# Performance work log

Measured on AMD Instinct MI355X. Metric: run time of the kernel, lower is better.

The kernel has to match this reference:

```python
import jax, jax.numpy as jnp
import numpy as np

B, C, H, W = 32, 3, 224, 224
P = 14            # n_patches per side
PS = H // P       # 16
D = 768           # embed_size
NH = 12           # heads
DH = D // NH      # 64
L = 12            # n_blocks
FF = 4 * D
OUT = 1000
S = P * P + 1     # 197 tokens


def positional_encoding(seq_len, d):
    i = jnp.arange(seq_len, dtype=jnp.float32)[:, None]
    j = jnp.arange(d, dtype=jnp.float32)[None, :]
    je = jnp.where(j % 2 == 0, j, j - 1)
    ang = i / jnp.power(10000.0, je / d)
    return jnp.where(j % 2 == 0, jnp.sin(ang), jnp.cos(ang))


def layernorm(x, g, b, eps=1e-5):
    mu = jnp.mean(x, axis=-1, keepdims=True)
    var = jnp.var(x, axis=-1, keepdims=True)
    return (x - mu) * jax.lax.rsqrt(var + eps) * g + b


def setup_inputs() -> dict:
    key = jax.random.key(0)
    ks = jax.random.split(key, 20)
    s = 0.02
    inp = {
        'images': jax.random.normal(ks[0], (B, C, H, W), jnp.float32),
        'W_patch': jax.random.normal(ks[1], (D, C * PS * PS), jnp.float32) * s,
        'b_patch': jnp.zeros((D,), jnp.float32),
        'class_token': jax.random.uniform(ks[2], (1, D), jnp.float32),
        'ln1_g': jnp.ones((L, D), jnp.float32),
        'ln1_b': jnp.zeros((L, D), jnp.float32),
        'Wq': jax.random.normal(ks[3], (L, NH, DH, DH), jnp.float32) * s,
        'bq': jnp.zeros((L, NH, DH), jnp.float32),
        'Wk': jax.random.normal(ks[4], (L, NH, DH, DH), jnp.float32) * s,
        'bk': jnp.zeros((L, NH, DH), jnp.float32),
        'Wv': jax.random.normal(ks[5], (L, NH, DH, DH), jnp.float32) * s,
        'bv': jnp.zeros((L, NH, DH), jnp.float32),
        'ln2_g': jnp.ones((L, D), jnp.float32),
        'ln2_b': jnp.zeros((L, D), jnp.float32),
        'W1': jax.random.normal(ks[6], (L, FF, D), jnp.float32) * s,
        'b1': jnp.zeros((L, FF), jnp.float32),
        'W2': jax.random.normal(ks[7], (L, D, FF), jnp.float32) * s,
        'b2': jnp.zeros((L, D), jnp.float32),
        'Wo': jax.random.normal(ks[8], (OUT, D), jnp.float32) * s,
        'bo': jnp.zeros((OUT,), jnp.float32),
    }
    return inp


def reference(images, W_patch, b_patch, class_token, ln1_g, ln1_b,
              Wq, bq, Wk, bk, Wv, bv, ln2_g, ln2_b, W1, b1, W2, b2, Wo, bo):
    b = images.shape[0]
    # patch extraction: [B,C,P,ps,P,ps] -> [B,P*P, C*ps*ps] (flatten order C,h,w)
    patches = images.reshape(b, C, P, PS, P, PS).transpose(0, 2, 4, 1, 3, 5)
    patches = patches.reshape(b, P * P, C * PS * PS)
    tokens = patches @ W_patch.T + b_patch                     # [B, P^2, D]
    cls = jnp.broadcast_to(class_token[None], (b, 1, D))
    x = jnp.concatenate([cls, tokens], axis=1)                 # [B, S, D]
    x = x + positional_encoding(S, D)

    scale = 1.0 / jnp.sqrt(jnp.float32(DH))
    for l in range(L):
        h = layernorm(x, ln1_g[l], ln1_b[l])
        hh = h.reshape(b, S, NH, DH)
        q = jnp.einsum('bshd,hed->bshe', hh, Wq[l]) + bq[l]
        k = jnp.einsum('bshd,hed->bshe', hh, Wk[l]) + bk[l]
        v = jnp.einsum('bshd,hed->bshe', hh, Wv[l]) + bv[l]
        scores = jnp.einsum('bshe,bthe->bhst', q, k) * scale   # [B,H,S,S]
        attn = jax.nn.softmax(scores, axis=-1)
        o = jnp.einsum('bhst,bthe->bshe', attn, v).reshape(b, S, D)
        x = x + o
        h2 = layernorm(x, ln2_g[l], ln2_b[l])
        ff = jax.nn.gelu(h2 @ W1[l].T + b1[l], approximate=False) @ W2[l].T + b2[l]
        x = x + ff

    logits = x[:, 0] @ Wo.T + bo                               # [B, OUT]
    return jax.nn.softmax(logits, axis=-1)
```

## Files before the change

### kernel.cpp

```cpp
#include <hip/hip_runtime.h>
#include <math.h>

static constexpr int kB   = 32;
static constexpr int kC   = 3;
static constexpr int kH   = 224;
static constexpr int kW   = 224;
static constexpr int kP   = 14;
static constexpr int kPS  = 16;
static constexpr int kD   = 768;
static constexpr int kNH  = 12;
static constexpr int kDH  = 64;
static constexpr int kL   = 12;
static constexpr int kFF  = 3072;
static constexpr int kOUT = 1000;
static constexpr int kS   = 197;
static constexpr int kTOK = kB * kS;
static constexpr int kNP  = kP * kP;
static constexpr int kMP  = 6400;
static constexpr int kQKV = 3 * kD;

typedef unsigned short u16;
typedef __attribute__((ext_vector_type(4))) float f32x4;
typedef __attribute__((ext_vector_type(8))) short bf16x8;

__device__ __forceinline__ u16 f2bf(float x) {
    unsigned u = __float_as_uint(x);
    return (u16)((u + 0x7FFFu + ((u >> 16) & 1u)) >> 16);
}
__device__ __forceinline__ float bf2f(u16 x) {
    return __uint_as_float((unsigned)x << 16);
}
__device__ __forceinline__ void cp16_async(void* lds, const void* g) {
    __builtin_amdgcn_global_load_lds((const __attribute__((address_space(1))) unsigned*)g,
                                     (__attribute__((address_space(3))) unsigned*)lds,
                                     16, 0, 0);
}

__global__ void vit_posenc(float* __restrict__ pos) {
    int idx = blockIdx.x * 256 + threadIdx.x;
    if (idx >= kS * kD) return;
    int s = idx / kD, d = idx % kD;
    int je = d & ~1;
    double p = pow(10000.0, (double)je / (double)kD);
    float ang = (float)((double)s / p);
    pos[idx] = (d & 1) ? cosf(ang) : sinf(ang);
}

__global__ void vit_im2col_bf16(const float* __restrict__ img, u16* __restrict__ patches) {
    long idx = (long)blockIdx.x * 256 + threadIdx.x;
    if (idx >= (long)kMP * kD) return;
    int col = (int)(idx % kD);
    long rp = idx / kD;
    if (rp >= (long)kB * kNP) { patches[idx] = 0; return; }
    int p = (int)(rp % kNP), b = (int)(rp / kNP);
    int c = col >> 8;
    int rem = col & 255;
    int i = rem >> 4, j = rem & 15;
    int py = p / kP, px = p % kP;
    patches[idx] = f2bf(img[(((long)b * kC + c) * kH + py * kPS + i) * kW + px * kPS + j]);
}

__global__ void vit_assemble(const float* __restrict__ tokens, const float* __restrict__ cls,
                             const float* __restrict__ pos, float* __restrict__ x) {
    long idx = (long)blockIdx.x * 256 + threadIdx.x;
    if (idx >= (long)kMP * kD) return;
    int d = (int)(idx % kD);
    long bs = idx / kD;
    if (bs >= kTOK) { x[idx] = 0.0f; return; }
    int s = (int)(bs % kS);
    long b = bs / kS;
    float v = (s == 0) ? cls[d] : tokens[((long)b * kNP + (s - 1)) * kD + d];
    x[idx] = v + pos[s * kD + d];
}

__global__ void cast_bf16(const float* __restrict__ in, u16* __restrict__ out, long n4) {
    long i = (long)blockIdx.x * 256 + threadIdx.x;
    if (i >= n4) return;
    float4 v = *(const float4*)(in + i * 4);
    *(ushort4*)(out + i * 4) = make_ushort4(f2bf(v.x), f2bf(v.y), f2bf(v.z), f2bf(v.w));
}

__global__ void zero_u16(u16* __restrict__ p, long n) {
    long i = (long)blockIdx.x * 256 + threadIdx.x;
    if (i < n) p[i] = 0;
}

__global__ void build_whb(const float* __restrict__ Wq, const float* __restrict__ Wk,
                          const float* __restrict__ Wv, const float* __restrict__ bq,
                          const float* __restrict__ bk, const float* __restrict__ bv,
                          u16* __restrict__ Wh, float* __restrict__ bh) {
    int idx = blockIdx.x * 256 + threadIdx.x;
    if (idx >= kNH * 192 * 64) return;
    int d = idx & 63;
    int r = (idx >> 6) % 192;
    int h = idx / (192 * 64);
    int sec = r >> 6, e = r & 63;
    const float* W = (sec == 0) ? Wq : (sec == 1) ? Wk : Wv;
    Wh[idx] = f2bf(W[((h << 6) + e) * 64 + d]);
    if (d == 0) {
        const float* bs = (sec == 0) ? bq : (sec == 1) ? bk : bv;
        bh[h * 192 + r] = bs[(h << 6) + e];
    }
}

__global__ __launch_bounds__(256) void vit_ln(const float* __restrict__ x,
                                              const float* __restrict__ g,
                                              const float* __restrict__ b,
                                              u16* __restrict__ out) {
    long t = blockIdx.x;
    const float* xr = x + t * kD;
    int tid = threadIdx.x;
    float v0 = xr[tid], v1 = xr[tid + 256], v2 = xr[tid + 512];
    float s  = v0 + v1 + v2;
    float sq = v0 * v0 + v1 * v1 + v2 * v2;
    #pragma unroll
    for (int o = 32; o; o >>= 1) { s += __shfl_xor(s, o); sq += __shfl_xor(sq, o); }
    __shared__ float red[8];
    int wid = tid >> 6, lane = tid & 63;
    if (lane == 0) { red[wid] = s; red[4 + wid] = sq; }
    __syncthreads();
    s  = red[0] + red[1] + red[2] + red[3];
    sq = red[4] + red[5] + red[6] + red[7];
    float mu  = s * (1.0f / kD);
    float var = sq * (1.0f / kD) - mu * mu;
    float rs  = rsqrtf(var + 1e-5f);
    u16* orow = out + t * kD;
    orow[tid]       = f2bf((v0 - mu) * rs * g[tid]       + b[tid]);
    orow[tid + 256] = f2bf((v1 - mu) * rs * g[tid + 256] + b[tid + 256]);
    orow[tid + 512] = f2bf((v2 - mu) * rs * g[tid + 512] + b[tid + 512]);
}

template <int EPI>
__global__ __launch_bounds__(256) void mm_bt(const u16* __restrict__ A, int lda,
                                             const u16* __restrict__ B, int ldb,
                                             const float* __restrict__ bias,
                                             const float* X, void* Cout, int ldc, int K) {
    __shared__ __align__(16) u16 As[3][4096];
    __shared__ __align__(16) u16 Bs[3][4096];

    const int gx = gridDim.x, gy = gridDim.y;
    const int nwg = gx * gy;
    const int disp = blockIdx.y * gx + blockIdx.x;
    const int q8 = nwg >> 3, r8 = nwg & 7;
    const int xcd = disp & 7, lot = disp >> 3;
    const int work = (xcd < r8 ? xcd * (q8 + 1) : r8 * (q8 + 1) + (xcd - r8) * q8) + lot;
    const int row0 = (work / gy) << 7;
    const int col0 = (work % gy) << 7;

    const int tid  = threadIdx.x;
    const int lane = tid & 63;
    const int wm = ((tid >> 6) >> 1) << 6;
    const int wn = ((tid >> 6) & 1) << 6;
    const int lr = lane & 15, lhi = lane >> 4;

    const int srow = tid >> 2;
    const int sch  = (((tid & 3) ^ ((srow >> 1) & 3)) << 3);
    const u16* Ag = A + (long)(row0 + srow) * lda + sch;
    const u16* Bg = B + (long)(col0 + srow) * ldb + sch;
    const long Astep = 64L * lda, Bstep = 64L * ldb;
    const int ldst = tid << 3;

    f32x4 acc[4][4] = {};
    const int nk = K >> 5;

    auto stage = [&](int buf, int k0) {
        cp16_async(&As[buf][ldst],        Ag + k0);
        cp16_async(&As[buf][ldst + 2048], Ag + Astep + k0);
        cp16_async(&Bs[buf][ldst],        Bg + k0);
        cp16_async(&Bs[buf][ldst + 2048], Bg + Bstep + k0);
    };
    stage(0, 0);
    stage(1, 32);

    const int rch = (lhi ^ ((lr >> 1) & 3)) << 3;
    int cur = 0;
    for (int t = 0; t < nk; t++) {
        if (t + 1 < nk) asm volatile("s_waitcnt vmcnt(4)" ::: "memory");
        else            asm volatile("s_waitcnt vmcnt(0)" ::: "memory");
        __builtin_amdgcn_sched_barrier(0);
        __builtin_amdgcn_s_barrier();
        bf16x8 af[4], bfr[4];
        #pragma unroll
        for (int m = 0; m < 4; m++)
            af[m] = *(const bf16x8*)&As[cur][(wm + (m << 4) + lr) * 32 + rch];
        #pragma unroll
        for (int n = 0; n < 4; n++)
            bfr[n] = *(const bf16x8*)&Bs[cur][(wn + (n << 4) + lr) * 32 + rch];
        if (t + 2 < nk) {
            int nb = cur + 2; if (nb >= 3) nb -= 3;
            stage(nb, (t + 2) << 5);
        }
        #pragma unroll
        for (int m = 0; m < 4; m++)
            #pragma unroll
            for (int n = 0; n < 4; n++)
                acc[m][n] = __builtin_amdgcn_mfma_f32_16x16x32_bf16(af[m], bfr[n], acc[m][n], 0, 0, 0);
        __builtin_amdgcn_s_barrier();
        cur = (cur + 1 == 3) ? 0 : cur + 1;
    }

    const int r0 = wm + (lhi << 2);
    const int cb = wn + lr;
    #pragma unroll
    for (int n = 0; n < 4; n++) {
        const int cc = col0 + cb + (n << 4);
        const float bv = bias[cc];
        #pragma unroll
        for (int m = 0; m < 4; m++) {
            #pragma unroll
            for (int r = 0; r < 4; r++) {
                const long idx = (long)(row0 + r0 + (m << 4) + r) * ldc + cc;
                float v = acc[m][n][r] + bv;
                if (EPI == 1) {
                    v = 0.5f * v * (1.0f + erff(v * 0.70710678118654752f));
                    ((u16*)Cout)[idx] = f2bf(v);
                } else if (EPI == 2) {
                    ((float*)Cout)[idx] = v + X[idx];
                } else if (EPI == 3) {
                    ((u16*)Cout)[idx] = f2bf(v);
                } else {
                    ((float*)Cout)[idx] = v;
                }
            }
        }
    }
}

__global__ __launch_bounds__(256) void mm_qkv(const u16* __restrict__ hbm,
                                              const u16* __restrict__ Wh,
                                              const float* __restrict__ bh,
                                              u16* __restrict__ qkv) {
    const int h = blockIdx.y;
    const int row0 = blockIdx.x << 6;
    const int tid = threadIdx.x, lane = tid & 63, wave = tid >> 6;
    const int l15 = lane & 15, lhi = lane >> 4;
    const u16* Ab = hbm + h * kDH + (lhi << 3);
    const u16* Bb = Wh + (long)h * 192 * 64 + (lhi << 3);

    bf16x8 af[4][2];
    #pragma unroll
    for (int m = 0; m < 4; m++) {
        const u16* ap = Ab + (long)(row0 + (m << 4) + l15) * kD;
        af[m][0] = *(const bf16x8*)ap;
        af[m][1] = *(const bf16x8*)(ap + 32);
    }
    bf16x8 bfr[3][2];
    #pragma unroll
    for (int n = 0; n < 3; n++) {
        const u16* bp = Bb + (long)(wave * 48 + (n << 4) + l15) * 64;
        bfr[n][0] = *(const bf16x8*)bp;
        bfr[n][1] = *(const bf16x8*)(bp + 32);
    }
    f32x4 acc[4][3] = {};
    __builtin_amdgcn_s_setprio(1);
    #pragma unroll
    for (int m = 0; m < 4; m++)
        #pragma unroll
        for (int n = 0; n < 3; n++) {
            acc[m][n] = __builtin_amdgcn_mfma_f32_16x16x32_bf16(af[m][0], bfr[n][0], acc[m][n], 0, 0, 0);
            acc[m][n] = __builtin_amdgcn_mfma_f32_16x16x32_bf16(af[m][1], bfr[n][1], acc[m][n], 0, 0, 0);
        }
    __builtin_amdgcn_s_setprio(0);
    #pragma unroll
    for (int n = 0; n < 3; n++) {
        const int c = wave * 48 + (n << 4) + l15;
        const int sec = c >> 6, e = c & 63;
        const float bv = bh[h * 192 + c];
        const long gcol = (long)sec * kD + h * kDH + e;
        #pragma unroll
        for (int m = 0; m < 4; m++)
            #pragma unroll
            for (int i = 0; i < 4; i++) {
                const int r = row0 + (m << 4) + (lhi << 2) + i;
                qkv[(long)r * kQKV + gcol] = f2bf(acc[m][n][i] + bv);
            }
    }
}

__global__ __launch_bounds__(256) void vit_attn_fused(const u16* __restrict__ qkv,
                                                      float* __restrict__ x) {
    constexpr int SP = 224;
    constexpr int NT = 13;
    constexpr int LDP = 232;
    __shared__ u16 Plds[64][LDP];
    __shared__ u16 Vt[64][LDP];

    const int z = blockIdx.y, qt = blockIdx.x;
    const int b = z / kNH, h = z % kNH;
    const u16* base = qkv + (long)b * kS * kQKV;
    const u16* Qg = base + h * kDH;
    const u16* Kg = base + kD + h * kDH;
    const u16* Vg = base + 2 * kD + h * kDH;
    const int tid = threadIdx.x, lane = tid & 63, wave = tid >> 6;
    const int l15 = lane & 15, lhi = lane >> 4;

    for (int i = tid; i < (SP * kDH) / 4; i += 256) {
        int s  = i >> 4;
        int d0 = (i & 15) << 2;
        ushort4 v = *(const ushort4*)(Vg + (long)s * kQKV + d0);
        Vt[d0 + 0][s] = v.x; Vt[d0 + 1][s] = v.y;
        Vt[d0 + 2][s] = v.z; Vt[d0 + 3][s] = v.w;
    }

    const int qrow = (qt << 6) + (wave << 4) + l15;
    const u16* qrp = Qg + (long)qrow * kQKV + (lhi << 3);
    const bf16x8 qf0 = *(const bf16x8*)(qrp);
    const bf16x8 qf1 = *(const bf16x8*)(qrp + 32);

    f32x4 sc[NT];
    const u16* krp = Kg + (long)l15 * kQKV + (lhi << 3);
    __builtin_amdgcn_s_setprio(1);
    #pragma unroll
    for (int t = 0; t < NT; t++) {
        const u16* kp = krp + (long)(t << 4) * kQKV;
        bf16x8 kb0 = *(const bf16x8*)(kp);
        bf16x8 kb1 = *(const bf16x8*)(kp + 32);
        f32x4 a = {0.0f, 0.0f, 0.0f, 0.0f};
        a = __builtin_amdgcn_mfma_f32_16x16x32_bf16(qf0, kb0, a, 0, 0, 0);
        a = __builtin_amdgcn_mfma_f32_16x16x32_bf16(qf1, kb1, a, 0, 0, 0);
        sc[t] = a;
    }
    __builtin_amdgcn_s_setprio(0);

    float mx[4] = {-1e30f, -1e30f, -1e30f, -1e30f};
    #pragma unroll
    for (int t = 0; t < NT; t++) {
        const int c = (t << 4) + l15;
        #pragma unroll
        for (int q = 0; q < 4; q++) {
            float v = (c < kS) ? sc[t][q] * 0.125f : -1e30f;
            sc[t][q] = v;
            mx[q] = fmaxf(mx[q], v);
        }
    }
    #pragma unroll
    for (int o = 1; o < 16; o <<= 1)
        #pragma unroll
        for (int q = 0; q < 4; q++) mx[q] = fmaxf(mx[q], __shfl_xor(mx[q], o));
    float sum[4] = {0.0f, 0.0f, 0.0f, 0.0f};
    #pragma unroll
    for (int t = 0; t < NT; t++)
        #pragma unroll
        for (int q = 0; q < 4; q++) {
            float e = __expf(sc[t][q] - mx[q]);
            sc[t][q] = e;
            sum[q] += e;
        }
    #pragma unroll
    for (int o = 1; o < 16; o <<= 1)
        #pragma unroll
        for (int q = 0; q < 4; q++) sum[q] += __shfl_xor(sum[q], o);

    const int prow = (wave << 4) + (lhi << 2);
    #pragma unroll
    for (int t = 0; t < NT; t++)
        #pragma unroll
        for (int q = 0; q < 4; q++)
            Plds[prow + q][(t << 4) + l15] = f2bf(sc[t][q]);
    #pragma unroll
    for (int q = 0; q < 4; q++)
        Plds[prow + q][208 + l15] = 0;
    __syncthreads();

    f32x4 oacc[4] = {};
    const int arow = (wave << 4) + l15;
    const int koff = lhi << 3;
    __builtin_amdgcn_s_setprio(1);
    #pragma unroll
    for (int ks = 0; ks < 7; ks++) {
        bf16x8 pa = *(const bf16x8*)&Plds[arow][ks * 32 + koff];
        #pragma unroll
        for (int n = 0; n < 4; n++) {
            bf16x8 vb = *(const bf16x8*)&Vt[(n << 4) + l15][ks * 32 + koff];
            oacc[n] = __builtin_amdgcn_mfma_f32_16x16x32_bf16(pa, vb, oacc[n], 0, 0, 0);
        }
    }
    __builtin_amdgcn_s_setprio(0);

    const int orow0 = (qt << 6) + (wave << 4) + (lhi << 2);
    #pragma unroll
    for (int q = 0; q < 4; q++) {
        const int r = orow0 + q;
        if (r >= kS) continue;
        const float rinv = 1.0f / sum[q];
        float* xp = x + ((long)b * kS + r) * kD + h * kDH + l15;
        #pragma unroll
        for (int n = 0; n < 4; n++)
            xp[n << 4] += oacc[n][q] * rinv;
    }
}

template <int ACT, int RES>
__global__ __launch_bounds__(256) void vit_gemm(const float* __restrict__ A, long lda, long sAz,
                                                const float* __restrict__ B, long ldb, long sBz,
                                                const float* __restrict__ bias, long sbz,
                                                const float* __restrict__ R,
                                                float* __restrict__ C, long ldc, long sCz,
                                                int M, int N, int K) {
    __shared__ __align__(16) float As[16][64];
    __shared__ __align__(16) float Bs[16][64];
    long z = blockIdx.z;
    A += z * sAz;  B += z * sBz;  C += z * sCz;
    if (bias) bias += z * sbz;
    const float* Rp = nullptr;
    if (RES) Rp = R + z * sCz;

    int row0 = blockIdx.x * 64, col0 = blockIdx.y * 64;
    int tid = threadIdx.x;
    int lr = tid >> 2, lk = (tid & 3) << 2;
    int tm = tid >> 4, tn = tid & 15;
    float acc[4][4] = {};

    for (int k0 = 0; k0 < K; k0 += 16) {
        float4 a = {0, 0, 0, 0}, bb = {0, 0, 0, 0};
        int gr = row0 + lr;
        if (gr < M) a = *(const float4*)(A + (long)gr * lda + k0 + lk);
        int gc = col0 + lr;
        if (gc < N) bb = *(const float4*)(B + (long)gc * ldb + k0 + lk);
        __syncthreads();
        As[lk + 0][lr] = a.x;  As[lk + 1][lr] = a.y;  As[lk + 2][lr] = a.z;  As[lk + 3][lr] = a.w;
        Bs[lk + 0][lr] = bb.x; Bs[lk + 1][lr] = bb.y; Bs[lk + 2][lr] = bb.z; Bs[lk + 3][lr] = bb.w;
        __syncthreads();
        #pragma unroll
        for (int k = 0; k < 16; k++) {
            const float4 av = *reinterpret_cast<const float4*>(&As[k][tm << 2]);
            const float4 bv = *reinterpret_cast<const float4*>(&Bs[k][tn << 2]);
            float aa[4] = {av.x, av.y, av.z, av.w};
            float bw[4] = {bv.x, bv.y, bv.z, bv.w};
            #pragma unroll
            for (int i = 0; i < 4; i++)
                #pragma unroll
                for (int j = 0; j < 4; j++)
                    acc[i][j] = fmaf(aa[i], bw[j], acc[i][j]);
        }
    }
    #pragma unroll
    for (int i = 0; i < 4; i++) {
        int r = row0 + (tm << 2) + i;
        if (r >= M) continue;
        #pragma unroll
        for (int j = 0; j < 4; j++) {
            int c = col0 + (tn << 2) + j;
            if (c >= N) continue;
            float v = acc[i][j];
            if (bias) v += bias[c];
            if (ACT == 1) v = 0.5f * v * (1.0f + erff(v * 0.70710678118654752f));
            if (RES) v += Rp[(long)r * ldc + c];
            C[(long)r * ldc + c] = v;
        }
    }
}

__global__ __launch_bounds__(256) void vit_smout(const float* __restrict__ logits,
                                                 float* __restrict__ out) {
    int b = blockIdx.x;
    const float* p = logits + (long)b * kOUT;
    int tid = threadIdx.x;
    float v[4];
    float mx = -1e30f;
    #pragma unroll
    for (int i = 0; i < 4; i++) {
        int c = tid + (i << 8);
        v[i] = (c < kOUT) ? p[c] : -1e30f;
        mx = fmaxf(mx, v[i]);
    }
    #pragma unroll
    for (int o = 32; o; o >>= 1) mx = fmaxf(mx, __shfl_xor(mx, o));
    __shared__ float red[8];
    int wid = tid >> 6, lane = tid & 63;
    if (lane == 0) red[wid] = mx;
    __syncthreads();
    mx = fmaxf(fmaxf(red[0], red[1]), fmaxf(red[2], red[3]));
    float sum = 0.0f;
    #pragma unroll
    for (int i = 0; i < 4; i++) {
        int c = tid + (i << 8);
        if (c < kOUT) { v[i] = expf(v[i] - mx); sum += v[i]; }
    }
    #pragma unroll
    for (int o = 32; o; o >>= 1) sum += __shfl_xor(sum, o);
    __syncthreads();
    if (lane == 0) red[4 + wid] = sum;
    __syncthreads();
    sum = red[4] + red[5] + red[6] + red[7];
    float inv = 1.0f / sum;
    #pragma unroll
    for (int i = 0; i < 4; i++) {
        int c = tid + (i << 8);
        if (c < kOUT) out[(long)b * kOUT + c] = v[i] * inv;
    }
}

extern "C" void kernel_launch(void* const* d_in, const int* in_sizes, int n_in,
                              void* d_out, int out_size, void* d_ws, size_t ws_size,
                              hipStream_t stream) {
    (void)in_sizes; (void)n_in; (void)out_size; (void)ws_size;
    const float* images  = (const float*)d_in[0];
    const float* W_patch = (const float*)d_in[1];
    const float* b_patch = (const float*)d_in[2];
    const float* cls     = (const float*)d_in[3];
    const float* ln1_g   = (const float*)d_in[4];
    const float* ln1_b   = (const float*)d_in[5];
    const float* Wq      = (const float*)d_in[6];
    const float* bq      = (const float*)d_in[7];
    const float* Wk      = (const float*)d_in[8];
    const float* bk      = (const float*)d_in[9];
    const float* Wv      = (const float*)d_in[10];
    const float* bv      = (const float*)d_in[11];
    const float* ln2_g   = (const float*)d_in[12];
    const float* ln2_b   = (const float*)d_in[13];
    const float* W1      = (const float*)d_in[14];
    const float* b1      = (const float*)d_in[15];
    const float* W2      = (const float*)d_in[16];
    const float* b2      = (const float*)d_in[17];
    const float* Wo      = (const float*)d_in[18];
    const float* bo      = (const float*)d_in[19];

    char* wsB = (char*)d_ws;
    auto alloc = [&](size_t bytes) { char* p = wsB; wsB += (bytes + 255) & ~(size_t)255; return p; };
    float* pos    = (float*)alloc((size_t)kS * kD * 4);
    float* x      = (float*)alloc((size_t)kMP * kD * 4);
    u16*   hb     = (u16*)  alloc((size_t)kMP * kD * 2);
    u16*   qkvb   = (u16*)  alloc((size_t)kMP * kQKV * 2);
    u16*   ff1b   = (u16*)  alloc((size_t)kMP * kFF * 2);
    u16*   W1b    = (u16*)  alloc((size_t)kFF * kD * 2);
    u16*   W2b    = (u16*)  alloc((size_t)kFF * kD * 2);
    u16*   Whb    = (u16*)  alloc((size_t)kNH * 192 * 64 * 2);
    u16*   Wpb    = (u16*)  alloc((size_t)kD * kD * 2);
    float* bhb    = (float*)alloc((size_t)kNH * 192 * 4);
    float* logits = (float*)alloc((size_t)kB * kOUT * 4);
    float* tokens   = (float*)qkvb;
    u16*   patchesb = ff1b;

    vit_posenc<<<(kS * kD + 255) / 256, 256, 0, stream>>>(pos);
    vit_im2col_bf16<<<(int)(((long)kMP * kD) / 256), 256, 0, stream>>>(images, patchesb);
    cast_bf16<<<(kD * kD / 4 + 255) / 256, 256, 0, stream>>>(W_patch, Wpb, (long)kD * kD / 4);
    zero_u16<<<(96 * kD + 255) / 256, 256, 0, stream>>>(hb + (long)kTOK * kD, 96L * kD);
    mm_bt<0><<<dim3(kMP / 128, kD / 128), 256, 0, stream>>>(
        patchesb, kD, Wpb, kD, b_patch, nullptr, tokens, kD, kD);
    vit_assemble<<<(int)(((long)kMP * kD) / 256), 256, 0, stream>>>(tokens, cls, pos, x);

    for (int l = 0; l < kL; l++) {
        cast_bf16<<<(kFF * kD / 4 + 255) / 256, 256, 0, stream>>>(
            W1 + (long)l * kFF * kD, W1b, (long)kFF * kD / 4);
        cast_bf16<<<(kFF * kD / 4 + 255) / 256, 256, 0, stream>>>(
            W2 + (long)l * kFF * kD, W2b, (long)kFF * kD / 4);
        build_whb<<<(kNH * 192 * 64 + 255) / 256, 256, 0, stream>>>(
            Wq + (long)l * kNH * kDH * kDH, Wk + (long)l * kNH * kDH * kDH,
            Wv + (long)l * kNH * kDH * kDH, bq + (long)l * kNH * kDH,
            bk + (long)l * kNH * kDH, bv + (long)l * kNH * kDH, Whb, bhb);

        vit_ln<<<kTOK, 256, 0, stream>>>(x, ln1_g + (long)l * kD, ln1_b + (long)l * kD, hb);
        mm_qkv<<<dim3(kMP / 64, kNH), 256, 0, stream>>>(hb, Whb, bhb, qkvb);

        vit_attn_fused<<<dim3(4, kB * kNH), 256, 0, stream>>>(qkvb, x);

        vit_ln<<<kTOK, 256, 0, stream>>>(x, ln2_g + (long)l * kD, ln2_b + (long)l * kD, hb);
        mm_bt<1><<<dim3(kMP / 128, kFF / 128), 256, 0, stream>>>(
            hb, kD, W1b, kD, b1 + (long)l * kFF, nullptr, ff1b, kFF, kD);
        mm_bt<2><<<dim3(kMP / 128, kD / 128), 256, 0, stream>>>(
            ff1b, kFF, W2b, kFF, b2 + (long)l * kD, x, x, kD, kFF);
    }

    vit_gemm<0, 0><<<dim3(1, 16, 1), 256, 0, stream>>>(
        x, (long)kS * kD, 0, Wo, kD, 0, bo, 0, nullptr,
        logits, kOUT, 0, kB, kOUT, kD);
    vit_smout<<<kB, 256, 0, stream>>>(logits, (float*)d_out);
}
```

Baseline: 2.544 ms.

## Switch GEMM to double-buffered BK=64 tiles with 8-way XOR swizzle

The bf16 MFMA GEMM changes from a triple-buffered K-step of 32 to a double-buffered K-step of 64. Each stage now loads 64-element rows with an 8-chunk XOR swizzle, and each tile runs two MFMA k-halves. The aim is to halve the number of loop iterations and barriers and to issue larger asynchronous loads per stage. In exchange, prefetch depth drops from two tiles to one, and LDS use per block rises, which could reduce occupancy or expose global-load latency.

```diff
diff --git a/kernel.cpp b/kernel.cpp
--- a/kernel.cpp
+++ b/kernel.cpp
@@ -135,8 +135,8 @@
                                              const u16* __restrict__ B, int ldb,
                                              const float* __restrict__ bias,
                                              const float* X, void* Cout, int ldc, int K) {
-    __shared__ __align__(16) u16 As[3][4096];
-    __shared__ __align__(16) u16 Bs[3][4096];
+    __shared__ __align__(16) u16 As[2][8192];
+    __shared__ __align__(16) u16 Bs[2][8192];
 
     const int gx = gridDim.x, gy = gridDim.y;
     const int nwg = gx * gy;
@@ -153,50 +153,60 @@
     const int wn = ((tid >> 6) & 1) << 6;
     const int lr = lane & 15, lhi = lane >> 4;
 
-    const int srow = tid >> 2;
-    const int sch  = (((tid & 3) ^ ((srow >> 1) & 3)) << 3);
-    const u16* Ag = A + (long)(row0 + srow) * lda + sch;
-    const u16* Bg = B + (long)(col0 + srow) * ldb + sch;
-    const long Astep = 64L * lda, Bstep = 64L * ldb;
+    const int srow = tid >> 3;
+    const int sc   = (((tid & 7) ^ (srow & 7)) << 3);
+    const u16* Ag = A + (long)(row0 + srow) * lda + sc;
+    const u16* Bg = B + (long)(col0 + srow) * ldb + sc;
+    const long Astep = 32L * lda, Bstep = 32L * ldb;
     const int ldst = tid << 3;
-
-    f32x4 acc[4][4] = {};
-    const int nk = K >> 5;
 
     auto stage = [&](int buf, int k0) {
         cp16_async(&As[buf][ldst],        Ag + k0);
         cp16_async(&As[buf][ldst + 2048], Ag + Astep + k0);
+        cp16_async(&As[buf][ldst + 4096], Ag + 2 * Astep + k0);
+        cp16_async(&As[buf][ldst + 6144], Ag + 3 * Astep + k0);
         cp16_async(&Bs[buf][ldst],        Bg + k0);
         cp16_async(&Bs[buf][ldst + 2048], Bg + Bstep + k0);
+        cp16_async(&Bs[buf][ldst + 4096], Bg + 2 * Bstep + k0);
+        cp16_async(&Bs[buf][ldst + 6144], Bg + 3 * Bstep + k0);
     };
+
+    f32x4 acc[4][4] = {};
+    const int nk = K >> 6;
     stage(0, 0);
-    stage(1, 32);
-
-    const int rch = (lhi ^ ((lr >> 1) & 3)) << 3;
-    int cur = 0;
+
     for (int t = 0; t < nk; t++) {
-        if (t + 1 < nk) asm volatile("s_waitcnt vmcnt(4)" ::: "memory");
-        else            asm volatile("s_waitcnt vmcnt(0)" ::: "memory");
+        const int cur = t & 1;
+        if (t + 1 < nk) {
+            stage(cur ^ 1, (t + 1) << 6);
+            asm volatile("s_waitcnt vmcnt(8)" ::: "memory");
+        } else {
+            asm volatile("s_waitcnt vmcnt(0)" ::: "memory");
+        }
         __builtin_amdgcn_sched_barrier(0);
         __builtin_amdgcn_s_barrier();
-        bf16x8 af[4], bfr[4];
-        #pragma unroll
-        for (int m = 0; m < 4; m++)
-            af[m] = *(const bf16x8*)&As[cur][(wm + (m << 4) + lr) * 32 + rch];
-        #pragma unroll
-        for (int n = 0; n < 4; n++)
-            bfr[n] = *(const bf16x8*)&Bs[cur][(wn + (n << 4) + lr) * 32 + rch];
-        if (t + 2 < nk) {
-            int nb = cur + 2; if (nb >= 3) nb -= 3;
-            stage(nb, (t + 2) << 5);
-        }
-        #pragma unroll
-        for (int m = 0; m < 4; m++)
+        #pragma unroll
+        for (int kh = 0; kh < 2; kh++) {
+            bf16x8 af[4], bfr[4];
             #pragma unroll
-            for (int n = 0; n < 4; n++)
-                acc[m][n] = __builtin_amdgcn_mfma_f32_16x16x32_bf16(af[m], bfr[n], acc[m][n], 0, 0, 0);
+            for (int m = 0; m < 4; m++) {
+                const int R = wm + (m << 4) + lr;
+                af[m] = *(const bf16x8*)&As[cur][R * 64 + ((((kh << 2) + lhi) ^ (R & 7)) << 3)];
+            }
+            #pragma unroll
+            for (int n = 0; n < 4; n++) {
+                const int R = wn + (n << 4) + lr;
+                bfr[n] = *(const bf16x8*)&Bs[cur][R * 64 + ((((kh << 2) + lhi) ^ (R & 7)) << 3)];
+            }
+            #pragma unroll
+            for (int m = 0; m < 4; m++)
+                #pragma unroll
+                for (int n = 0; n < 4; n++)
+                    acc[m][n] = __builtin_amdgcn_mfma_f32_16x16x32_bf16(af[m], bfr[n], acc[m][n], 0, 0, 0);
+        }
+        asm volatile("s_waitcnt lgkmcnt(0)" ::: "memory");
+        __builtin_amdgcn_sched_barrier(0);
         __builtin_amdgcn_s_barrier();
-        cur = (cur + 1 == 3) ? 0 : cur + 1;
     }
 
     const int r0 = wm + (lhi << 2);
```

Result: slower. 2.691 ms (median of 4 runs) (+5.8%).
